# Performance work log

Hardware: AMD Instinct MI355X
Metric: run time of the kernel (lower is better)

The kernel has to match this reference:

```python
import jax, jax.numpy as jnp
import numpy as np
from jax import lax

TOP_K = 8
EPS = 1e-12


def l2_normalize(x, axis):
    sq = jnp.sum(x * x, axis=axis, keepdims=True)
    return x * lax.rsqrt(jnp.maximum(sq, EPS))


def setup_inputs() -> dict:
    key = jax.random.key(0)
    k1, k2, k3, k4 = jax.random.split(key, 4)
    B, N, C = 256, 197, 768
    POOL, LEN = 1024, 8
    x_embed = jax.random.normal(k1, (B, N, C), dtype=jnp.float32)
    prompt = jax.random.uniform(k2, (POOL, LEN, C), dtype=jnp.float32, minval=-1.0, maxval=1.0)
    prompt_key = jax.random.uniform(k3, (POOL, C), dtype=jnp.float32, minval=-1.0, maxval=1.0)
    # kaiming_normal fan_out: std = sqrt(2 / fan_out)
    proj_w = jax.random.normal(k4, (C, C), dtype=jnp.float32) * np.sqrt(2.0 / C).astype(np.float32)
    proj_b = jnp.zeros((C,), dtype=jnp.float32)
    return {"x_embed": x_embed, "prompt": prompt, "prompt_key": prompt_key,
            "proj_w": proj_w, "proj_b": proj_b}


def reference(x_embed, prompt, prompt_key, proj_w, proj_b):
    B = x_embed.shape[0]
    # embedding_key == 'mean'
    x_mean = jnp.mean(x_embed, axis=1)                     # [B, C]
    prompt_norm = l2_normalize(prompt_key, axis=1)         # [P, C]
    x_norm = l2_normalize(x_mean, axis=1)                  # [B, C]
    similarity = x_norm @ prompt_norm.T                    # [B, P]
    _, idx = lax.top_k(similarity, TOP_K)                  # [B, K]
    # gather prompts: [B, K, L, C] -> [B, K*L, C]
    bp = prompt[idx]
    Bk, K, L, C = bp.shape
    batched_prompt = bp.reshape(Bk, K * L, C)
    # projection + residual (dropout in eval mode = identity)
    batched_prompt = batched_prompt @ proj_w.T + proj_b + batched_prompt
    # key loss term
    batched_key_norm = prompt_norm[idx]                    # [B, K, C]
    reduce_sim = jnp.sum(batched_key_norm * x_norm[:, None, :]) / B
    prompted = jnp.concatenate([x_embed[:, :1, :], batched_prompt, x_embed[:, 1:, :]], axis=1)
    return prompted, reduce_sim
```

## Files before the change

kernel.cpp:

```cpp
#include <hip/hip_runtime.h>
#include <float.h>
#include <math.h>

#define B_    256
#define N_    197
#define C_    768
#define POOL_ 1024
#define LEN_  8
#define TOPK_ 8
#define PROWS (POOL_*LEN_)
#define OUTROWS 261

typedef __attribute__((ext_vector_type(8))) short short8_t;
typedef __attribute__((ext_vector_type(4))) float f32x4;

static const size_t OFF_XMEAN = 0;
static const size_t OFF_SIM   = 786432;
static const size_t OFF_IDX   = 1835008;
static const size_t OFF_ACC   = 1843200;
static const size_t OFF_ABF   = 1843456;
static const size_t OFF_WBF   = 14426368;
static const size_t OFF_PROJ  = 15606016;

__device__ __forceinline__ unsigned short f2bf(float f) {
    unsigned int u = __float_as_uint(f);
    u += 0x7fffu + ((u >> 16) & 1u);
    return (unsigned short)(u >> 16);
}

__global__ __launch_bounds__(256) void kA(const float* __restrict__ x,
                                          const float* __restrict__ prompt,
                                          const float* __restrict__ projw,
                                          float* __restrict__ out,
                                          float* __restrict__ xmean,
                                          unsigned short* __restrict__ Abf,
                                          unsigned short* __restrict__ Wbf,
                                          float* __restrict__ accum) {
    const int bid = blockIdx.x, t = threadIdx.x;
    if (bid == 0 && t == 0) accum[0] = 0.0f;
    if (bid < B_ * 3) {
        __shared__ f32x4 red[4][64];
        const int b = bid / 3, seg = bid % 3;
        const int r = t >> 6;
        const int c = t & 63;
        const int c4 = seg * 64 + c;
        const f32x4* xin  = (const f32x4*)x   + (size_t)b * (N_ * 192) + c4;
        f32x4*       outb = (f32x4*)out       + (size_t)b * (OUTROWS * 192) + c4;
        float sx = 0.f, sy = 0.f, sz = 0.f, sw = 0.f;
        #pragma unroll 7
        for (int n = r; n < 196; n += 4) {
            f32x4 v = __builtin_nontemporal_load(&xin[(size_t)n * 192]);
            sx += v.x; sy += v.y; sz += v.z; sw += v.w;
            int orow = (n == 0) ? 0 : (64 + n);
            __builtin_nontemporal_store(v, &outb[(size_t)orow * 192]);
        }
        if (r == 0) {
            f32x4 v = __builtin_nontemporal_load(&xin[(size_t)196 * 192]);
            sx += v.x; sy += v.y; sz += v.z; sw += v.w;
            __builtin_nontemporal_store(v, &outb[(size_t)260 * 192]);
        }
        f32x4 s; s.x = sx; s.y = sy; s.z = sz; s.w = sw;
        red[r][c] = s;
        __syncthreads();
        if (r == 0) {
            f32x4 a = red[0][c], b2 = red[1][c], c2 = red[2][c], d = red[3][c];
            const float inv = 1.0f / (float)N_;
            f32x4 m;
            m.x = (a.x + b2.x + c2.x + d.x) * inv;
            m.y = (a.y + b2.y + c2.y + d.y) * inv;
            m.z = (a.z + b2.z + c2.z + d.z) * inv;
            m.w = (a.w + b2.w + c2.w + d.w) * inv;
            ((f32x4*)xmean)[b * 192 + c4] = m;
        }
    } else {
        int i4 = (bid - B_ * 3) * 256 + t;
        float4 v; unsigned short* d;
        if (i4 < (PROWS * C_ / 4)) {
            v = ((const float4*)prompt)[i4];
            d = Abf + (size_t)i4 * 4;
        } else {
            int j4 = i4 - PROWS * C_ / 4;
            v = ((const float4*)projw)[j4];
            d = Wbf + (size_t)j4 * 4;
        }
        ushort4 o; o.x = f2bf(v.x); o.y = f2bf(v.y); o.z = f2bf(v.z); o.w = f2bf(v.w);
        *(ushort4*)d = o;
    }
}

__global__ __launch_bounds__(256) void kB(const unsigned short* __restrict__ A,
                                          const unsigned short* __restrict__ W,
                                          const float* __restrict__ bias,
                                          const float* __restrict__ resid,
                                          float* __restrict__ projout,
                                          const float* __restrict__ xmean,
                                          const float* __restrict__ pkey,
                                          float* __restrict__ sim) {
    __shared__ __align__(16) char smem[24576];
    const int tid = threadIdx.x;
    const int bid = blockIdx.x;

    if (bid < 768) {
        short (*As5)[64*32]  = (short (*)[64*32])(smem);
        short (*Bs5)[128*32] = (short (*)[128*32])(smem + 8192);
        const int m0 = (bid / 6) * 64, n0 = (bid % 6) * 128;
        const int wave = tid >> 6, lane = tid & 63;
        const int quad = lane >> 4, lr = lane & 15;
        const int srow = tid >> 2;
        const int scol = (tid & 3) * 8;

        f32x4 acc[4][2] = {};

        auto stage = [&](int buf, int kt) {
            const int k0 = kt * 32;
            __builtin_amdgcn_global_load_lds(
                (const __attribute__((address_space(1))) void*)&A[(size_t)(m0 + srow) * C_ + k0 + scol],
                (__attribute__((address_space(3))) void*)&As5[buf][srow*32 + scol], 16, 0, 0);
            __builtin_amdgcn_global_load_lds(
                (const __attribute__((address_space(1))) void*)&W[(size_t)(n0 + srow) * C_ + k0 + scol],
                (__attribute__((address_space(3))) void*)&Bs5[buf][srow*32 + scol], 16, 0, 0);
            __builtin_amdgcn_global_load_lds(
                (const __attribute__((address_space(1))) void*)&W[(size_t)(n0 + 64 + srow) * C_ + k0 + scol],
                (__attribute__((address_space(3))) void*)&Bs5[buf][(64 + srow)*32 + scol], 16, 0, 0);
        };
        auto compute = [&](int buf) {
            short8_t af[4], bf[2];
            #pragma unroll
            for (int i = 0; i < 4; ++i)
                af[i] = *(const short8_t*)&As5[buf][(i*16 + lr)*32 + quad*8];
            #pragma unroll
            for (int j = 0; j < 2; ++j)
                bf[j] = *(const short8_t*)&Bs5[buf][(wave*32 + j*16 + lr)*32 + quad*8];
            #pragma unroll
            for (int i = 0; i < 4; ++i)
                #pragma unroll
                for (int j = 0; j < 2; ++j)
                    acc[i][j] = __builtin_amdgcn_mfma_f32_16x16x32_bf16(af[i], bf[j], acc[i][j], 0, 0, 0);
        };

        stage(0, 0);
        __syncthreads();
        int cur = 0;
        for (int kt = 0; kt < 23; ++kt) {
            stage(cur ^ 1, kt + 1);
            compute(cur);
            __syncthreads();
            cur ^= 1;
        }
        compute(cur);

        #pragma unroll
        for (int j = 0; j < 2; ++j) {
            const int n = n0 + wave*32 + j*16 + lr;
            const float bn = bias[n];
            #pragma unroll
            for (int i = 0; i < 4; ++i) {
                const int mbase = m0 + i*16 + quad*4;
                #pragma unroll
                for (int r = 0; r < 4; ++r) {
                    const int m = mbase + r;
                    projout[(size_t)m * C_ + n] = acc[i][j][r] + bn + resid[(size_t)m * C_ + n];
                }
            }
        }
    } else {
        float (*As3)[36] = (float (*)[36])(smem);
        float (*Bs3)[36] = (float (*)[36])(smem + 4608);
        float* sqA  = (float*)(smem + 9216);
        float* sqB  = (float*)(smem + 10240);
        float* invs = (float*)(smem + 11264);
        const int q = bid - 768;
        const int m0 = (q >> 5) * 32, n0 = (q & 31) * 32;
        const int t = tid;
        const int lrow = t >> 3, lc = (t & 7) * 4;
        const int ty = t >> 4, tx = t & 15;
        float a00 = 0.f, a01 = 0.f, a10 = 0.f, a11 = 0.f;
        float sqa = 0.f, sqb = 0.f;
        float4 va = *(const float4*)&xmean[(size_t)(m0 + lrow) * C_ + lc];
        float4 vb = *(const float4*)&pkey [(size_t)(n0 + lrow) * C_ + lc];
        for (int k0 = 0; k0 < C_; k0 += 32) {
            __syncthreads();
            *(float4*)&As3[lrow][lc] = va;
            *(float4*)&Bs3[lrow][lc] = vb;
            sqa += va.x*va.x + va.y*va.y + va.z*va.z + va.w*va.w;
            sqb += vb.x*vb.x + vb.y*vb.y + vb.z*vb.z + vb.w*vb.w;
            __syncthreads();
            if (k0 + 32 < C_) {
                va = *(const float4*)&xmean[(size_t)(m0 + lrow) * C_ + k0 + 32 + lc];
                vb = *(const float4*)&pkey [(size_t)(n0 + lrow) * C_ + k0 + 32 + lc];
            }
            #pragma unroll
            for (int kk = 0; kk < 32; kk += 4) {
                float4 A0 = *(const float4*)&As3[ty*2][kk];
                float4 A1 = *(const float4*)&As3[ty*2+1][kk];
                float4 B0 = *(const float4*)&Bs3[tx*2][kk];
                float4 B1 = *(const float4*)&Bs3[tx*2+1][kk];
                a00 += A0.x*B0.x; a00 += A0.y*B0.y; a00 += A0.z*B0.z; a00 += A0.w*B0.w;
                a01 += A0.x*B1.x; a01 += A0.y*B1.y; a01 += A0.z*B1.z; a01 += A0.w*B1.w;
                a10 += A1.x*B0.x; a10 += A1.y*B0.y; a10 += A1.z*B0.z; a10 += A1.w*B0.w;
                a11 += A1.x*B1.x; a11 += A1.y*B1.y; a11 += A1.z*B1.z; a11 += A1.w*B1.w;
            }
        }
        sqA[lrow*8 + (t & 7)] = sqa;
        sqB[lrow*8 + (t & 7)] = sqb;
        __syncthreads();
        if (t < 64) {
            const float* s = (t < 32) ? sqA : sqB;
            const int rr = t & 31;
            float tot = 0.f;
            #pragma unroll
            for (int j = 0; j < 8; ++j) tot += s[rr*8 + j];
            invs[t] = 1.0f / sqrtf(fmaxf(tot, 1e-12f));
        }
        __syncthreads();
        const float im0 = invs[ty*2], im1 = invs[ty*2 + 1];
        const float ip0 = invs[32 + tx*2], ip1 = invs[32 + tx*2 + 1];
        sim[(size_t)(m0 + ty*2    ) * POOL_ + n0 + tx*2    ] = a00 * im0 * ip0;
        sim[(size_t)(m0 + ty*2    ) * POOL_ + n0 + tx*2 + 1] = a01 * im0 * ip1;
        sim[(size_t)(m0 + ty*2 + 1) * POOL_ + n0 + tx*2    ] = a10 * im1 * ip0;
        sim[(size_t)(m0 + ty*2 + 1) * POOL_ + n0 + tx*2 + 1] = a11 * im1 * ip1;
    }
}

__global__ __launch_bounds__(256) void kC1_topk(const float* __restrict__ sim,
                                                int* __restrict__ idx,
                                                float* __restrict__ accum) {
    __shared__ float vals[POOL_];
    __shared__ float wv[4];
    __shared__ int   wi[4];
    const int b = blockIdx.x, t = threadIdx.x;
    const int wave = t >> 6;
    #pragma unroll
    for (int i = 0; i < 4; ++i) vals[t + 256*i] = sim[(size_t)b * POOL_ + t + 256*i];
    __syncthreads();
    float sumv = 0.0f;
    for (int k = 0; k < TOPK_; ++k) {
        float bv = -FLT_MAX; int bi = POOL_;
        #pragma unroll
        for (int i = 0; i < 4; ++i) {
            int n = t + 256*i;
            float v = vals[n];
            if (v > bv) { bv = v; bi = n; }
        }
        #pragma unroll
        for (int off = 32; off > 0; off >>= 1) {
            float v2 = __shfl_down(bv, off);
            int   i2 = __shfl_down(bi, off);
            if (v2 > bv || (v2 == bv && i2 < bi)) { bv = v2; bi = i2; }
        }
        if ((t & 63) == 0) { wv[wave] = bv; wi[wave] = bi; }
        __syncthreads();
        if (t == 0) {
            float fv = wv[0]; int fi = wi[0];
            #pragma unroll
            for (int w = 1; w < 4; ++w) {
                float v2 = wv[w]; int i2 = wi[w];
                if (v2 > fv || (v2 == fv && i2 < fi)) { fv = v2; fi = i2; }
            }
            idx[b*TOPK_ + k] = fi;
            sumv += fv;
            vals[fi] = -FLT_MAX;
        }
        __syncthreads();
    }
    if (t == 0) atomicAdd(accum, sumv);
}

__global__ __launch_bounds__(256) void kC2_gather(const float* __restrict__ projall,
                                                  const int* __restrict__ idx,
                                                  const float* __restrict__ accum,
                                                  float* __restrict__ out) {
    int row = blockIdx.x * 4 + (threadIdx.x >> 6);
    int t = threadIdx.x & 63;
    int b = row >> 6, j = row & 63;
    int k = j >> 3, l = j & 7;
    int p = idx[b * TOPK_ + k];
    const f32x4* src = (const f32x4*)projall + (size_t)(p * LEN_ + l) * 192;
    f32x4* dst = (f32x4*)out + (size_t)(b * OUTROWS + 1 + j) * 192;
    __builtin_nontemporal_store(src[t],       &dst[t]);
    __builtin_nontemporal_store(src[t + 64],  &dst[t + 64]);
    __builtin_nontemporal_store(src[t + 128], &dst[t + 128]);
    if (row == 0 && t == 0)
        out[(size_t)B_ * OUTROWS * C_] = accum[0] * (1.0f / (float)B_);
}

extern "C" void kernel_launch(void* const* d_in, const int* in_sizes, int n_in,
                              void* d_out, int out_size, void* d_ws, size_t ws_size,
                              hipStream_t stream) {
    const float* x_embed = (const float*)d_in[0];
    const float* prompt  = (const float*)d_in[1];
    const float* pkey    = (const float*)d_in[2];
    const float* projw   = (const float*)d_in[3];
    const float* projb   = (const float*)d_in[4];
    float* out = (float*)d_out;
    char* ws = (char*)d_ws;

    float*          xmean   = (float*)(ws + OFF_XMEAN);
    float*          sim     = (float*)(ws + OFF_SIM);
    int*            idxp    = (int*)(ws + OFF_IDX);
    float*          acc     = (float*)(ws + OFF_ACC);
    unsigned short* Abf     = (unsigned short*)(ws + OFF_ABF);
    unsigned short* Wbf     = (unsigned short*)(ws + OFF_WBF);
    float*          projall = (float*)(ws + OFF_PROJ);

    const int convBlocks = (PROWS * C_ / 4 + 768 * 768 / 4) / 256;
    kA<<<B_ * 3 + convBlocks, 256, 0, stream>>>(x_embed, prompt, projw,
                                                out, xmean, Abf, Wbf, acc);
    kB<<<1024, 256, 0, stream>>>(Abf, Wbf, projb, prompt, projall,
                                 xmean, pkey, sim);
    kC1_topk<<<B_, 256, 0, stream>>>(sim, idxp, acc);
    kC2_gather<<<B_ * 64 / 4, 256, 0, stream>>>(projall, idxp, acc, out);
}
```

Before: 413.7 us.

## Scatter GEMM results directly to output via inverted top-k index lists

The GEMM over all prompt rows now runs after top-k. Its epilogue scatters each computed row straight into every output slot that selected that prompt, using per-prompt counters and entry lists built with atomics in the top-k kernel. This removes the fp32 intermediate projection buffer (write plus gather read) and the separate gather kernel. The x_embed copy into the output moves from the mean kernel into the similarity kernel, which re-reads x_embed, and write order is now nondeterministic with skewed per-prompt fan-out.

Result: no change. 411.0 us (-0.7%).

```diff
diff --git a/kernel.cpp b/kernel.cpp
--- a/kernel.cpp
+++ b/kernel.cpp
@@ -16,11 +16,11 @@
 
 static const size_t OFF_XMEAN = 0;
 static const size_t OFF_SIM   = 786432;
-static const size_t OFF_IDX   = 1835008;
-static const size_t OFF_ACC   = 1843200;
-static const size_t OFF_ABF   = 1843456;
-static const size_t OFF_WBF   = 14426368;
-static const size_t OFF_PROJ  = 15606016;
+static const size_t OFF_ACC   = 1835008;
+static const size_t OFF_CNT   = 1835264;
+static const size_t OFF_ENT   = 1839360;
+static const size_t OFF_ABF   = 2887936;
+static const size_t OFF_WBF   = 15470848;
 
 __device__ __forceinline__ unsigned short f2bf(float f) {
     unsigned int u = __float_as_uint(f);
@@ -31,33 +31,28 @@
 __global__ __launch_bounds__(256) void kA(const float* __restrict__ x,
                                           const float* __restrict__ prompt,
                                           const float* __restrict__ projw,
-                                          float* __restrict__ out,
                                           float* __restrict__ xmean,
                                           unsigned short* __restrict__ Abf,
                                           unsigned short* __restrict__ Wbf,
+                                          int* __restrict__ cnt,
                                           float* __restrict__ accum) {
     const int bid = blockIdx.x, t = threadIdx.x;
-    if (bid == 0 && t == 0) accum[0] = 0.0f;
     if (bid < B_ * 3) {
         __shared__ f32x4 red[4][64];
         const int b = bid / 3, seg = bid % 3;
         const int r = t >> 6;
         const int c = t & 63;
         const int c4 = seg * 64 + c;
-        const f32x4* xin  = (const f32x4*)x   + (size_t)b * (N_ * 192) + c4;
-        f32x4*       outb = (f32x4*)out       + (size_t)b * (OUTROWS * 192) + c4;
+        const f32x4* xin = (const f32x4*)x + (size_t)b * (N_ * 192) + c4;
         float sx = 0.f, sy = 0.f, sz = 0.f, sw = 0.f;
         #pragma unroll 7
         for (int n = r; n < 196; n += 4) {
-            f32x4 v = __builtin_nontemporal_load(&xin[(size_t)n * 192]);
+            f32x4 v = xin[(size_t)n * 192];
             sx += v.x; sy += v.y; sz += v.z; sw += v.w;
-            int orow = (n == 0) ? 0 : (64 + n);
-            __builtin_nontemporal_store(v, &outb[(size_t)orow * 192]);
         }
         if (r == 0) {
-            f32x4 v = __builtin_nontemporal_load(&xin[(size_t)196 * 192]);
+            f32x4 v = xin[(size_t)196 * 192];
             sx += v.x; sy += v.y; sz += v.z; sw += v.w;
-            __builtin_nontemporal_store(v, &outb[(size_t)260 * 192]);
         }
         f32x4 s; s.x = sx; s.y = sy; s.z = sz; s.w = sw;
         red[r][c] = s;
@@ -72,8 +67,11 @@
             m.w = (a.w + b2.w + c2.w + d.w) * inv;
             ((f32x4*)xmean)[b * 192 + c4] = m;
         }
+    } else if (bid == B_ * 3) {
+        ((f32x4*)cnt)[t] = f32x4{0.f, 0.f, 0.f, 0.f};
+        if (t == 0) accum[0] = 0.0f;
     } else {
-        int i4 = (bid - B_ * 3) * 256 + t;
+        int i4 = (bid - (B_ * 3 + 1)) * 256 + t;
         float4 v; unsigned short* d;
         if (i4 < (PROWS * C_ / 4)) {
             v = ((const float4*)prompt)[i4];
@@ -88,90 +86,20 @@
     }
 }
 
-__global__ __launch_bounds__(256) void kB(const unsigned short* __restrict__ A,
-                                          const unsigned short* __restrict__ W,
-                                          const float* __restrict__ bias,
-                                          const float* __restrict__ resid,
-                                          float* __restrict__ projout,
-                                          const float* __restrict__ xmean,
+__global__ __launch_bounds__(256) void kS(const float* __restrict__ xmean,
                                           const float* __restrict__ pkey,
-                                          float* __restrict__ sim) {
-    __shared__ __align__(16) char smem[24576];
-    const int tid = threadIdx.x;
-    const int bid = blockIdx.x;
-
-    if (bid < 768) {
-        short (*As5)[64*32]  = (short (*)[64*32])(smem);
-        short (*Bs5)[128*32] = (short (*)[128*32])(smem + 8192);
-        const int m0 = (bid / 6) * 64, n0 = (bid % 6) * 128;
-        const int wave = tid >> 6, lane = tid & 63;
-        const int quad = lane >> 4, lr = lane & 15;
-        const int srow = tid >> 2;
-        const int scol = (tid & 3) * 8;
-
-        f32x4 acc[4][2] = {};
-
-        auto stage = [&](int buf, int kt) {
-            const int k0 = kt * 32;
-            __builtin_amdgcn_global_load_lds(
-                (const __attribute__((address_space(1))) void*)&A[(size_t)(m0 + srow) * C_ + k0 + scol],
-                (__attribute__((address_space(3))) void*)&As5[buf][srow*32 + scol], 16, 0, 0);
-            __builtin_amdgcn_global_load_lds(
-                (const __attribute__((address_space(1))) void*)&W[(size_t)(n0 + srow) * C_ + k0 + scol],
-                (__attribute__((address_space(3))) void*)&Bs5[buf][srow*32 + scol], 16, 0, 0);
-            __builtin_amdgcn_global_load_lds(
-                (const __attribute__((address_space(1))) void*)&W[(size_t)(n0 + 64 + srow) * C_ + k0 + scol],
-                (__attribute__((address_space(3))) void*)&Bs5[buf][(64 + srow)*32 + scol], 16, 0, 0);
-        };
-        auto compute = [&](int buf) {
-            short8_t af[4], bf[2];
-            #pragma unroll
-            for (int i = 0; i < 4; ++i)
-                af[i] = *(const short8_t*)&As5[buf][(i*16 + lr)*32 + quad*8];
-            #pragma unroll
-            for (int j = 0; j < 2; ++j)
-                bf[j] = *(const short8_t*)&Bs5[buf][(wave*32 + j*16 + lr)*32 + quad*8];
-            #pragma unroll
-            for (int i = 0; i < 4; ++i)
-                #pragma unroll
-                for (int j = 0; j < 2; ++j)
-                    acc[i][j] = __builtin_amdgcn_mfma_f32_16x16x32_bf16(af[i], bf[j], acc[i][j], 0, 0, 0);
-        };
-
-        stage(0, 0);
-        __syncthreads();
-        int cur = 0;
-        for (int kt = 0; kt < 23; ++kt) {
-            stage(cur ^ 1, kt + 1);
-            compute(cur);
-            __syncthreads();
-            cur ^= 1;
-        }
-        compute(cur);
-
-        #pragma unroll
-        for (int j = 0; j < 2; ++j) {
-            const int n = n0 + wave*32 + j*16 + lr;
-            const float bn = bias[n];
-            #pragma unroll
-            for (int i = 0; i < 4; ++i) {
-                const int mbase = m0 + i*16 + quad*4;
-                #pragma unroll
-                for (int r = 0; r < 4; ++r) {
-                    const int m = mbase + r;
-                    projout[(size_t)m * C_ + n] = acc[i][j][r] + bn + resid[(size_t)m * C_ + n];
-                }
-            }
-        }
-    } else {
-        float (*As3)[36] = (float (*)[36])(smem);
-        float (*Bs3)[36] = (float (*)[36])(smem + 4608);
-        float* sqA  = (float*)(smem + 9216);
-        float* sqB  = (float*)(smem + 10240);
-        float* invs = (float*)(smem + 11264);
-        const int q = bid - 768;
-        const int m0 = (q >> 5) * 32, n0 = (q & 31) * 32;
-        const int t = tid;
+                                          float* __restrict__ sim,
+                                          const float* __restrict__ x,
+                                          float* __restrict__ out) {
+    __shared__ float As3[32][36];
+    __shared__ float Bs3[32][36];
+    __shared__ float sqA[32*8];
+    __shared__ float sqB[32*8];
+    __shared__ float invs[64];
+    const int bid = blockIdx.x, t = threadIdx.x;
+
+    if (bid < 256) {
+        const int m0 = (bid >> 5) * 32, n0 = (bid & 31) * 32;
         const int lrow = t >> 3, lc = (t & 7) * 4;
         const int ty = t >> 4, tx = t & 15;
         float a00 = 0.f, a01 = 0.f, a10 = 0.f, a11 = 0.f;
@@ -219,15 +147,34 @@
         sim[(size_t)(m0 + ty*2    ) * POOL_ + n0 + tx*2 + 1] = a01 * im0 * ip1;
         sim[(size_t)(m0 + ty*2 + 1) * POOL_ + n0 + tx*2    ] = a10 * im1 * ip0;
         sim[(size_t)(m0 + ty*2 + 1) * POOL_ + n0 + tx*2 + 1] = a11 * im1 * ip1;
-    }
-}
-
-__global__ __launch_bounds__(256) void kC1_topk(const float* __restrict__ sim,
-                                                int* __restrict__ idx,
-                                                float* __restrict__ accum) {
+    } else {
+        const int cb = bid - 256;
+        const int b = cb / 3, seg = cb % 3;
+        const int r = t >> 6, c = t & 63;
+        const int c4 = seg * 64 + c;
+        const f32x4* xin  = (const f32x4*)x   + (size_t)b * (N_ * 192) + c4;
+        f32x4*       outb = (f32x4*)out       + (size_t)b * (OUTROWS * 192) + c4;
+        #pragma unroll 7
+        for (int n = r; n < 196; n += 4) {
+            f32x4 v = xin[(size_t)n * 192];
+            int orow = (n == 0) ? 0 : (64 + n);
+            __builtin_nontemporal_store(v, &outb[(size_t)orow * 192]);
+        }
+        if (r == 0) {
+            f32x4 v = xin[(size_t)196 * 192];
+            __builtin_nontemporal_store(v, &outb[(size_t)260 * 192]);
+        }
+    }
+}
+
+__global__ __launch_bounds__(256) void kT(const float* __restrict__ sim,
+                                          int* __restrict__ cnt,
+                                          int* __restrict__ entries,
+                                          float* __restrict__ accum) {
     __shared__ float vals[POOL_];
     __shared__ float wv[4];
     __shared__ int   wi[4];
+    __shared__ int   sidx[TOPK_];
     const int b = blockIdx.x, t = threadIdx.x;
     const int wave = t >> 6;
     #pragma unroll
@@ -257,31 +204,109 @@
                 float v2 = wv[w]; int i2 = wi[w];
                 if (v2 > fv || (v2 == fv && i2 < fi)) { fv = v2; fi = i2; }
             }
-            idx[b*TOPK_ + k] = fi;
+            sidx[k] = fi;
             sumv += fv;
             vals[fi] = -FLT_MAX;
         }
         __syncthreads();
     }
+    if (t < TOPK_) {
+        const int p = sidx[t];
+        const int pos = atomicAdd(&cnt[p], 1);
+        entries[(p << 8) + pos] = (b << 3) | t;
+    }
     if (t == 0) atomicAdd(accum, sumv);
 }
 
-__global__ __launch_bounds__(256) void kC2_gather(const float* __restrict__ projall,
-                                                  const int* __restrict__ idx,
-                                                  const float* __restrict__ accum,
-                                                  float* __restrict__ out) {
-    int row = blockIdx.x * 4 + (threadIdx.x >> 6);
-    int t = threadIdx.x & 63;
-    int b = row >> 6, j = row & 63;
-    int k = j >> 3, l = j & 7;
-    int p = idx[b * TOPK_ + k];
-    const f32x4* src = (const f32x4*)projall + (size_t)(p * LEN_ + l) * 192;
-    f32x4* dst = (f32x4*)out + (size_t)(b * OUTROWS + 1 + j) * 192;
-    __builtin_nontemporal_store(src[t],       &dst[t]);
-    __builtin_nontemporal_store(src[t + 64],  &dst[t + 64]);
-    __builtin_nontemporal_store(src[t + 128], &dst[t + 128]);
-    if (row == 0 && t == 0)
+__global__ __launch_bounds__(256) void kG(const unsigned short* __restrict__ A,
+                                          const unsigned short* __restrict__ W,
+                                          const float* __restrict__ bias,
+                                          const float* __restrict__ resid,
+                                          const int* __restrict__ cnt,
+                                          const int* __restrict__ entries,
+                                          const float* __restrict__ accum,
+                                          float* __restrict__ out) {
+    __shared__ short As5[2][64*32];
+    __shared__ short Bs5[2][128*32];
+    const int tid = threadIdx.x;
+    const int bid = blockIdx.x;
+    if (bid == 0 && tid == 0)
         out[(size_t)B_ * OUTROWS * C_] = accum[0] * (1.0f / (float)B_);
+
+    const int m0 = (bid / 6) * 64, n0 = (bid % 6) * 128;
+    const int wave = tid >> 6, lane = tid & 63;
+    const int quad = lane >> 4, lr = lane & 15;
+    const int srow = tid >> 2;
+    const int scol = (tid & 3) * 8;
+
+    f32x4 acc[4][2] = {};
+
+    auto stage = [&](int buf, int kt) {
+        const int k0 = kt * 32;
+        __builtin_amdgcn_global_load_lds(
+            (const __attribute__((address_space(1))) void*)&A[(size_t)(m0 + srow) * C_ + k0 + scol],
+            (__attribute__((address_space(3))) void*)&As5[buf][srow*32 + scol], 16, 0, 0);
+        __builtin_amdgcn_global_load_lds(
+            (const __attribute__((address_space(1))) void*)&W[(size_t)(n0 + srow) * C_ + k0 + scol],
+            (__attribute__((address_space(3))) void*)&Bs5[buf][srow*32 + scol], 16, 0, 0);
+        __builtin_amdgcn_global_load_lds(
+            (const __attribute__((address_space(1))) void*)&W[(size_t)(n0 + 64 + srow) * C_ + k0 + scol],
+            (__attribute__((address_space(3))) void*)&Bs5[buf][(64 + srow)*32 + scol], 16, 0, 0);
+    };
+    auto compute = [&](int buf) {
+        short8_t af[4], bf[2];
+        #pragma unroll
+        for (int i = 0; i < 4; ++i)
+            af[i] = *(const short8_t*)&As5[buf][(i*16 + lr)*32 + quad*8];
+        #pragma unroll
+        for (int j = 0; j < 2; ++j)
+            bf[j] = *(const short8_t*)&Bs5[buf][(wave*32 + j*16 + lr)*32 + quad*8];
+        #pragma unroll
+        for (int i = 0; i < 4; ++i)
+            #pragma unroll
+            for (int j = 0; j < 2; ++j)
+                acc[i][j] = __builtin_amdgcn_mfma_f32_16x16x32_bf16(af[i], bf[j], acc[i][j], 0, 0, 0);
+    };
+
+    stage(0, 0);
+    __syncthreads();
+    int cur = 0;
+    for (int kt = 0; kt < 23; ++kt) {
+        stage(cur ^ 1, kt + 1);
+        compute(cur);
+        __syncthreads();
+        cur ^= 1;
+    }
+    compute(cur);
+
+    const float bn0 = bias[n0 + wave*32 + lr];
+    const float bn1 = bias[n0 + wave*32 + 16 + lr];
+    const int ncol = n0 + wave*32 + lr;
+    #pragma unroll
+    for (int i = 0; i < 4; ++i) {
+        const int m  = m0 + i*16 + quad*4;
+        const int p  = m >> 3;
+        const int lb = m & 7;
+        const int c  = cnt[p];
+        if (c != 0) {
+            float vals[2][4];
+            #pragma unroll
+            for (int r = 0; r < 4; ++r) {
+                vals[0][r] = acc[i][0][r] + bn0 + resid[(size_t)(m + r) * C_ + ncol];
+                vals[1][r] = acc[i][1][r] + bn1 + resid[(size_t)(m + r) * C_ + ncol + 16];
+            }
+            for (int h = 0; h < c; ++h) {
+                const int bk = entries[(p << 8) + h];
+                const size_t obase =
+                    (size_t)((bk >> 3) * OUTROWS + 1 + (bk & 7) * 8 + lb) * C_ + ncol;
+                #pragma unroll
+                for (int r = 0; r < 4; ++r) {
+                    out[obase + (size_t)r * C_]      = vals[0][r];
+                    out[obase + (size_t)r * C_ + 16] = vals[1][r];
+                }
+            }
+        }
+    }
 }
 
 extern "C" void kernel_launch(void* const* d_in, const int* in_sizes, int n_in,
@@ -297,17 +322,16 @@
 
     float*          xmean   = (float*)(ws + OFF_XMEAN);
     float*          sim     = (float*)(ws + OFF_SIM);
-    int*            idxp    = (int*)(ws + OFF_IDX);
     float*          acc     = (float*)(ws + OFF_ACC);
+    int*            cnt     = (int*)(ws + OFF_CNT);
+    int*            ent     = (int*)(ws + OFF_ENT);
     unsigned short* Abf     = (unsigned short*)(ws + OFF_ABF);
     unsigned short* Wbf     = (unsigned short*)(ws + OFF_WBF);
-    float*          projall = (float*)(ws + OFF_PROJ);
 
     const int convBlocks = (PROWS * C_ / 4 + 768 * 768 / 4) / 256;
-    kA<<<B_ * 3 + convBlocks, 256, 0, stream>>>(x_embed, prompt, projw,
-                                                out, xmean, Abf, Wbf, acc);
-    kB<<<1024, 256, 0, stream>>>(Abf, Wbf, projb, prompt, projall,
-                                 xmean, pkey, sim);
-    kC1_topk<<<B_, 256, 0, stream>>>(sim, idxp, acc);
-    kC2_gather<<<B_ * 64 / 4, 256, 0, stream>>>(projall, idxp, acc, out);
-}
+    kA<<<B_ * 3 + 1 + convBlocks, 256, 0, stream>>>(x_embed, prompt, projw,
+                                                    xmean, Abf, Wbf, cnt, acc);
+    kS<<<1024, 256, 0, stream>>>(xmean, pkey, sim, x_embed, out);
+    kT<<<B_, 256, 0, stream>>>(sim, cnt, ent, acc);
+    kG<<<768, 256, 0, stream>>>(Abf, Wbf, projb, prompt, cnt, ent, acc, out);
+}
```
